# Kernel tuning notes

Measured on AMD Instinct MI355X. Metric: run time of the kernel, lower is better.

## Reference

```python
import jax, jax.numpy as jnp
import numpy as np

TEM = 0.5
BN_EPS = 1e-5
ROWS, IN_FEA, OUT_FEA = 16384, 512, 128


def setup_inputs() -> dict:
    key = jax.random.key(0)
    ks = jax.random.split(key, 3)
    doc_fea = jax.random.normal(ks[0], (ROWS, IN_FEA), dtype=jnp.float32)
    W1 = jax.random.normal(ks[1], (IN_FEA, OUT_FEA), dtype=jnp.float32) * 0.02
    b1 = jnp.zeros((OUT_FEA,), dtype=jnp.float32)
    gamma = jnp.ones((OUT_FEA,), dtype=jnp.float32)
    beta = jnp.zeros((OUT_FEA,), dtype=jnp.float32)
    W2 = jax.random.normal(ks[2], (OUT_FEA, OUT_FEA), dtype=jnp.float32) * 0.02
    b2 = jnp.zeros((OUT_FEA,), dtype=jnp.float32)
    return {"doc_fea": doc_fea, "W1": W1, "b1": b1, "gamma": gamma,
            "beta": beta, "W2": W2, "b2": b2}


def _l2_normalize(x):
    # matches torch F.normalize(dim=1, eps=1e-12)
    n = jnp.linalg.norm(x, axis=1, keepdims=True)
    return x / jnp.maximum(n, 1e-12)


def _half_loss(a, b):
    # rows of a, b are unit-norm, so cosine sim == matmul
    between = jnp.exp(a @ b.T / TEM)          # [N, N]
    refl = jnp.exp(a @ a.T / TEM)             # [N, N]
    pos = jnp.diagonal(between)
    denom = refl.sum(axis=1) + between.sum(axis=1) - jnp.diagonal(refl)
    return -jnp.log(pos / denom)


def reference(doc_fea, W1, b1, gamma, beta, W2, b2):
    # projector: Linear -> BatchNorm1d (training stats) -> ReLU -> Linear
    h = doc_fea @ W1 + b1
    mu = h.mean(axis=0)
    var = h.var(axis=0)  # biased variance, as used by torch BN normalization
    h = (h - mu) * jax.lax.rsqrt(var + BN_EPS) * gamma + beta
    h = jax.nn.relu(h)
    out = h @ W2 + b2
    out = _l2_normalize(out)
    # original: out_1 = out[indices where i%2!=0], out_2 = out[i%2==0]
    out_1 = out[1::2]
    out_2 = out[0::2]
    l1 = _half_loss(out_1, out_2)
    l2 = _half_loss(out_2, out_1)
    loss = (l1 + l2) * 0.5
    return loss.mean()
```

## Files before the change

kernel.cpp:

```cpp
#include <hip/hip_runtime.h>

typedef __attribute__((ext_vector_type(8))) short short8;
typedef __attribute__((ext_vector_type(4))) float f32x4;

typedef const __attribute__((address_space(1))) unsigned int as1_u32;
typedef __attribute__((address_space(3))) unsigned int as3_u32;

#define E2f   7.38905609893065f
#define OSCALE 1.69864357f

#if __has_builtin(__builtin_amdgcn_exp2f)
#define EXP2(x) __builtin_amdgcn_exp2f(x)
#else
#define EXP2(x) exp2f(x)
#endif

__device__ inline unsigned short f2bf(float f){
    union { float f; unsigned int u; } x; x.f = f;
    unsigned int u = x.u;
    return (unsigned short)((u + 0x7fffu + ((u >> 16) & 1u)) >> 16);
}

__device__ inline short8 pack8(float4 a, float4 b){
    short8 t;
    t[0]=(short)f2bf(a.x); t[1]=(short)f2bf(a.y); t[2]=(short)f2bf(a.z); t[3]=(short)f2bf(a.w);
    t[4]=(short)f2bf(b.x); t[5]=(short)f2bf(b.y); t[6]=(short)f2bf(b.z); t[7]=(short)f2bf(b.w);
    return t;
}

__global__ __launch_bounds__(256) void k_prep(const float* __restrict__ W1, const float* __restrict__ W2,
                                              short* __restrict__ W1T, short* __restrict__ W2T){
    int idx = blockIdx.x*256 + threadIdx.x;
    if(idx < 512*128){
        int n = idx >> 9, k = idx & 511;
        W1T[idx] = (short)f2bf(W1[k*128 + n]);
    } else {
        int i2 = idx - 512*128;
        int n = i2 >> 7, k = i2 & 127;
        W2T[i2] = (short)f2bf(W2[k*128 + n]);
    }
}

__global__ __launch_bounds__(256) void k_gemm1(const float* __restrict__ doc, const float* __restrict__ b1,
                                               const short* __restrict__ W1T, float* __restrict__ h,
                                               float* __restrict__ bsum, float* __restrict__ bsq){
    int bid = blockIdx.x;
    int tid = threadIdx.x;
    int w = tid >> 6, l = tid & 63, lr = l & 15, lk = l >> 4;
    int rowA = bid*64 + w*16 + lr;

    short8 a[16];
    const float* dp = doc + rowA*512 + lk*8;
    #pragma unroll
    for(int c=0;c<16;c++){
        float4 f0 = *(const float4*)(dp + c*32);
        float4 f1 = *(const float4*)(dp + c*32 + 4);
        a[c] = pack8(f0, f1);
    }

    f32x4 acc[8];
    #pragma unroll
    for(int ct=0; ct<8; ct++) acc[ct] = (f32x4){0.f,0.f,0.f,0.f};

    const short* wb = W1T + lr*512 + lk*8;
    #pragma unroll
    for(int c=0;c<16;c++){
        #pragma unroll
        for(int ct=0; ct<8; ct++){
            short8 b = *(const short8*)(wb + ct*16*512 + c*32);
            acc[ct] = __builtin_amdgcn_mfma_f32_16x16x32_bf16(a[c], b, acc[ct], 0,0,0);
        }
    }

    __shared__ float lds_s[4][128];
    __shared__ float lds_q[4][128];
    int rowD = bid*64 + w*16 + lk*4;
    #pragma unroll
    for(int ct=0; ct<8; ct++){
        float bb = b1[ct*16 + lr];
        float s = 0.f, q = 0.f;
        #pragma unroll
        for(int r=0;r<4;r++){
            float v = acc[ct][r] + bb;
            h[(rowD + r)*128 + ct*16 + lr] = v;
            s += v; q += v*v;
        }
        s += __shfl_xor(s,16); s += __shfl_xor(s,32);
        q += __shfl_xor(q,16); q += __shfl_xor(q,32);
        if(lk==0){ lds_s[w][ct*16+lr] = s; lds_q[w][ct*16+lr] = q; }
    }
    __syncthreads();
    if(tid < 128){
        float S = lds_s[0][tid]+lds_s[1][tid]+lds_s[2][tid]+lds_s[3][tid];
        float Q = lds_q[0][tid]+lds_q[1][tid]+lds_q[2][tid]+lds_q[3][tid];
        bsum[bid*128 + tid] = S;
        bsq [bid*128 + tid] = Q;
    }
}

__global__ __launch_bounds__(128) void k_bnfin(const float* __restrict__ bsum, const float* __restrict__ bsq,
                                               const float* __restrict__ gamma, const float* __restrict__ beta,
                                               float* __restrict__ bnA, float* __restrict__ bnB){
    int c = threadIdx.x;
    float S=0.f, Q=0.f;
    for(int b=0;b<256;b++){ S += bsum[b*128+c]; Q += bsq[b*128+c]; }
    float mu = S * (1.0f/16384.0f);
    float var = Q * (1.0f/16384.0f) - mu*mu;
    float A = gamma[c] * rsqrtf(var + 1e-5f);
    bnA[c] = A;
    bnB[c] = beta[c] - mu*A;
}

__global__ __launch_bounds__(256) void k_gemm2(const float* __restrict__ h, const short* __restrict__ W2T,
                                               const float* __restrict__ bnA, const float* __restrict__ bnB,
                                               const float* __restrict__ b2,
                                               short* __restrict__ o1s, short* __restrict__ o2s,
                                               float* __restrict__ dvec){
    int bid = blockIdx.x;
    int tid = threadIdx.x;
    int w = tid >> 6, l = tid & 63, lr = l & 15, lk = l >> 4;
    int rowA = bid*64 + w*16 + lr;

    short8 a[4];
    const float* hp = h + rowA*128 + lk*8;
    #pragma unroll
    for(int c=0;c<4;c++){
        float4 h0 = *(const float4*)(hp + c*32);
        float4 h1 = *(const float4*)(hp + c*32 + 4);
        float4 A0 = *(const float4*)(bnA + c*32 + lk*8);
        float4 A1 = *(const float4*)(bnA + c*32 + lk*8 + 4);
        float4 B0 = *(const float4*)(bnB + c*32 + lk*8);
        float4 B1 = *(const float4*)(bnB + c*32 + lk*8 + 4);
        float4 v0, v1;
        v0.x = fmaxf(h0.x*A0.x + B0.x, 0.f); v0.y = fmaxf(h0.y*A0.y + B0.y, 0.f);
        v0.z = fmaxf(h0.z*A0.z + B0.z, 0.f); v0.w = fmaxf(h0.w*A0.w + B0.w, 0.f);
        v1.x = fmaxf(h1.x*A1.x + B1.x, 0.f); v1.y = fmaxf(h1.y*A1.y + B1.y, 0.f);
        v1.z = fmaxf(h1.z*A1.z + B1.z, 0.f); v1.w = fmaxf(h1.w*A1.w + B1.w, 0.f);
        a[c] = pack8(v0, v1);
    }

    f32x4 acc[8];
    #pragma unroll
    for(int ct=0; ct<8; ct++) acc[ct] = (f32x4){0.f,0.f,0.f,0.f};
    const short* wb = W2T + lr*128 + lk*8;
    #pragma unroll
    for(int c=0;c<4;c++){
        #pragma unroll
        for(int ct=0; ct<8; ct++){
            short8 b = *(const short8*)(wb + ct*16*128 + c*32);
            acc[ct] = __builtin_amdgcn_mfma_f32_16x16x32_bf16(a[c], b, acc[ct], 0,0,0);
        }
    }

    #pragma unroll
    for(int ct=0; ct<8; ct++){
        float bb = b2[ct*16 + lr];
        #pragma unroll
        for(int r=0;r<4;r++) acc[ct][r] += bb;
    }
    float n2[4] = {0.f,0.f,0.f,0.f};
    #pragma unroll
    for(int ct=0; ct<8; ct++){
        #pragma unroll
        for(int r=0;r<4;r++) n2[r] += acc[ct][r]*acc[ct][r];
    }
    #pragma unroll
    for(int r=0;r<4;r++){
        n2[r] += __shfl_xor(n2[r],1); n2[r] += __shfl_xor(n2[r],2);
        n2[r] += __shfl_xor(n2[r],4); n2[r] += __shfl_xor(n2[r],8);
    }
    float sc[4];
    #pragma unroll
    for(int r=0;r<4;r++) sc[r] = 1.0f / fmaxf(sqrtf(n2[r]), 1e-12f);
    #pragma unroll
    for(int ct=0; ct<8; ct++){
        #pragma unroll
        for(int r=0;r<4;r++) acc[ct][r] *= sc[r];
    }
    float dp0 = 0.f, dp1 = 0.f;
    #pragma unroll
    for(int ct=0; ct<8; ct++){
        dp0 += acc[ct][0]*acc[ct][1];
        dp1 += acc[ct][2]*acc[ct][3];
    }
    dp0 += __shfl_xor(dp0,1); dp0 += __shfl_xor(dp0,2); dp0 += __shfl_xor(dp0,4); dp0 += __shfl_xor(dp0,8);
    dp1 += __shfl_xor(dp1,1); dp1 += __shfl_xor(dp1,2); dp1 += __shfl_xor(dp1,4); dp1 += __shfl_xor(dp1,8);
    int r0 = bid*64 + w*16 + lk*4;
    if(lr==0){
        dvec[(r0>>1)    ] = dp0;
        dvec[(r0>>1) + 1] = dp1;
    }
    #pragma unroll
    for(int ct=0; ct<8; ct++){
        #pragma unroll
        for(int r=0;r<4;r++){
            int grow = r0 + r;
            int col  = ct*16 + lr;
            short bits = (short)f2bf(acc[ct][r] * OSCALE);
            if(grow & 1) o1s[(grow>>1)*128 + col] = bits;
            else         o2s[(grow>>1)*128 + col] = bits;
        }
    }
}

__global__ __launch_bounds__(256) void k_sim(const short* __restrict__ o1s, const short* __restrict__ o2s,
                                             float* __restrict__ r11p, float* __restrict__ r22p,
                                             float* __restrict__ r12p, float* __restrict__ c12p){
    int bx = blockIdx.x, by = blockIdx.y, pz = blockIdx.z;
    const short* A = (pz==1) ? o2s : o1s;
    const short* B = (pz==0) ? o1s : o2s;
    float* rowp = (pz==0) ? r11p : (pz==1 ? r22p : r12p);
    const bool colsum = (pz==2);

    int tid = threadIdx.x;
    int w = tid>>6, l = tid&63, lr = l&15, lk = l>>4;

    __shared__ __align__(16) short lds[2][8192];
    __shared__ float cs_lds[2][4][64];

    short8 a[2][4];
    {
        const short* ap = A + (bx*128 + w*32 + lr)*128 + lk*8;
        #pragma unroll
        for(int rt=0;rt<2;rt++)
            #pragma unroll
            for(int c=0;c<4;c++)
                a[rt][c] = *(const short8*)(ap + rt*2048 + c*32);
    }

    int sb[4];
    #pragma unroll
    for(int c=0;c<4;c++) sb[c] = lr*256 + ((((c*4+lk) ^ (lr&7)))<<4);

    const short* gsrc[4];
    #pragma unroll
    for(int i=0;i<4;i++){
        int chunk = i*4 + w;
        int row = chunk*4 + (l>>4);
        int col16 = (l&15) ^ (row&7);
        gsrc[i] = B + (by*512 + row)*128 + col16*8;
    }

    #pragma unroll
    for(int i=0;i<4;i++){
        __builtin_amdgcn_global_load_lds((as1_u32*)gsrc[i],
            (as3_u32*)(&lds[0][(i*4+w)*512]), 16, 0, 0);
        gsrc[i] += 8192;
    }
    asm volatile("s_waitcnt vmcnt(0)" ::: "memory");
    __syncthreads();

    float rs[2][4] = {{0.f,0.f,0.f,0.f},{0.f,0.f,0.f,0.f}};
    int buf = 0;
    const char* lbase = (const char*)&lds[0][0];

    for(int t=0;t<8;t++){
        if(t<7){
            #pragma unroll
            for(int i=0;i<4;i++){
                __builtin_amdgcn_global_load_lds((as1_u32*)gsrc[i],
                    (as3_u32*)(&lds[buf^1][(i*4+w)*512]), 16, 0, 0);
                gsrc[i] += 8192;
            }
        }
        const char* lb = lbase + buf*16384;
        #pragma unroll
        for(int jt=0;jt<4;jt++){
            short8 b0 = *(const short8*)(lb + jt*4096 + sb[0]);
            short8 b1 = *(const short8*)(lb + jt*4096 + sb[1]);
            short8 b2 = *(const short8*)(lb + jt*4096 + sb[2]);
            short8 b3 = *(const short8*)(lb + jt*4096 + sb[3]);
            f32x4 c0 = (f32x4){0.f,0.f,0.f,0.f};
            f32x4 c1 = (f32x4){0.f,0.f,0.f,0.f};
            c0 = __builtin_amdgcn_mfma_f32_16x16x32_bf16(a[0][0], b0, c0,0,0,0);
            c1 = __builtin_amdgcn_mfma_f32_16x16x32_bf16(a[1][0], b0, c1,0,0,0);
            c0 = __builtin_amdgcn_mfma_f32_16x16x32_bf16(a[0][1], b1, c0,0,0,0);
            c1 = __builtin_amdgcn_mfma_f32_16x16x32_bf16(a[1][1], b1, c1,0,0,0);
            c0 = __builtin_amdgcn_mfma_f32_16x16x32_bf16(a[0][2], b2, c0,0,0,0);
            c1 = __builtin_amdgcn_mfma_f32_16x16x32_bf16(a[1][2], b2, c1,0,0,0);
            c0 = __builtin_amdgcn_mfma_f32_16x16x32_bf16(a[0][3], b3, c0,0,0,0);
            c1 = __builtin_amdgcn_mfma_f32_16x16x32_bf16(a[1][3], b3, c1,0,0,0);
            float e00 = EXP2(c0[0]), e01 = EXP2(c0[1]), e02 = EXP2(c0[2]), e03 = EXP2(c0[3]);
            float e10 = EXP2(c1[0]), e11 = EXP2(c1[1]), e12 = EXP2(c1[2]), e13 = EXP2(c1[3]);
            rs[0][0]+=e00; rs[0][1]+=e01; rs[0][2]+=e02; rs[0][3]+=e03;
            rs[1][0]+=e10; rs[1][1]+=e11; rs[1][2]+=e12; rs[1][3]+=e13;
            if(colsum){
                float cv = ((e00+e01)+(e02+e03)) + ((e10+e11)+(e12+e13));
                cv += __shfl_xor(cv,16); cv += __shfl_xor(cv,32);
                if(lk==0) cs_lds[t&1][w][jt*16+lr] = cv;
            }
        }
        asm volatile("s_waitcnt vmcnt(0)" ::: "memory");
        __syncthreads();
        if(colsum && tid < 64){
            float v = cs_lds[t&1][0][tid]+cs_lds[t&1][1][tid]
                    + cs_lds[t&1][2][tid]+cs_lds[t&1][3][tid];
            c12p[bx*8192 + by*512 + t*64 + tid] = v;
        }
        buf ^= 1;
    }

    #pragma unroll
    for(int rt=0;rt<2;rt++){
        #pragma unroll
        for(int r=0;r<4;r++){
            rs[rt][r] += __shfl_xor(rs[rt][r],1);
            rs[rt][r] += __shfl_xor(rs[rt][r],2);
            rs[rt][r] += __shfl_xor(rs[rt][r],4);
            rs[rt][r] += __shfl_xor(rs[rt][r],8);
        }
        if(lr==0){
            float4 v; v.x=rs[rt][0]; v.y=rs[rt][1]; v.z=rs[rt][2]; v.w=rs[rt][3];
            *(float4*)(rowp + by*8192 + bx*128 + w*32 + rt*16 + lk*4) = v;
        }
    }
}

__global__ __launch_bounds__(256) void k_loss1(const float* __restrict__ r11, const float* __restrict__ r12,
                                               const float* __restrict__ r22, const float* __restrict__ c12,
                                               const float* __restrict__ dvec, float* __restrict__ lpart){
    int i = blockIdx.x*256 + threadIdx.x;
    float s11=0.f, s12=0.f, s22=0.f, s21=0.f;
    #pragma unroll
    for(int s=0;s<16;s++){
        s11 += r11[s*8192+i]; s12 += r12[s*8192+i]; s22 += r22[s*8192+i];
    }
    #pragma unroll
    for(int s=0;s<64;s++) s21 += c12[s*8192+i];
    float d1 = s11 - E2f + s12;
    float d2 = s22 - E2f + s21;
    float loss = 0.5f*(logf(d1)+logf(d2)) - 2.0f*dvec[i];
    loss += __shfl_xor(loss,1);  loss += __shfl_xor(loss,2);  loss += __shfl_xor(loss,4);
    loss += __shfl_xor(loss,8);  loss += __shfl_xor(loss,16); loss += __shfl_xor(loss,32);
    __shared__ float lds[4];
    if((threadIdx.x & 63) == 0) lds[threadIdx.x >> 6] = loss;
    __syncthreads();
    if(threadIdx.x == 0) lpart[blockIdx.x] = lds[0]+lds[1]+lds[2]+lds[3];
}

__global__ __launch_bounds__(64) void k_loss2(const float* __restrict__ lpart, float* __restrict__ out){
    if(threadIdx.x == 0){
        float s = 0.f;
        for(int i=0;i<32;i++) s += lpart[i];
        out[0] = s * (1.0f/8192.0f);
    }
}

extern "C" void kernel_launch(void* const* d_in, const int* in_sizes, int n_in,
                              void* d_out, int out_size, void* d_ws, size_t ws_size,
                              hipStream_t stream){
    (void)in_sizes; (void)n_in; (void)out_size; (void)ws_size;
    const float* doc   = (const float*)d_in[0];
    const float* W1    = (const float*)d_in[1];
    const float* b1    = (const float*)d_in[2];
    const float* gamma = (const float*)d_in[3];
    const float* beta  = (const float*)d_in[4];
    const float* W2    = (const float*)d_in[5];
    const float* b2    = (const float*)d_in[6];
    float* out = (float*)d_out;

    char* ws = (char*)d_ws;
    float* h     = (float*)(ws + 0);
    float* c12p  = (float*)(ws + 0);
    float* r11p  = (float*)(ws + 2097152);
    float* r22p  = (float*)(ws + 2621440);
    float* r12p  = (float*)(ws + 3145728);
    short* W1T   = (short*)(ws + 8388608);
    short* W2T   = (short*)(ws + 8519680);
    short* o1s   = (short*)(ws + 8552448);
    short* o2s   = (short*)(ws + 10649600);
    float* dvec  = (float*)(ws + 12746752);
    float* bnA   = (float*)(ws + 12779520);
    float* bnB   = (float*)(ws + 12780032);
    float* bsum  = (float*)(ws + 12780544);
    float* bsq   = (float*)(ws + 12911616);
    float* lpart = (float*)(ws + 13042688);

    k_prep <<<320, 256, 0, stream>>>(W1, W2, W1T, W2T);
    k_gemm1<<<256, 256, 0, stream>>>(doc, b1, W1T, h, bsum, bsq);
    k_bnfin<<<1, 128, 0, stream>>>(bsum, bsq, gamma, beta, bnA, bnB);
    k_gemm2<<<256, 256, 0, stream>>>(h, W2T, bnA, bnB, b2, o1s, o2s, dvec);
    dim3 sg(64, 16, 3);
    k_sim  <<<sg, 256, 0, stream>>>(o1s, o2s, r11p, r22p, r12p, c12p);
    k_loss1<<<32, 256, 0, stream>>>(r11p, r12p, r22p, c12p, dvec, lpart);
    k_loss2<<<1, 64, 0, stream>>>(lpart, out);
}
```

Before: 129.1 us.

## Exploit symmetry of self-similarity blocks and restructure GEMM launches and sim pipeline

The similarity kernel now skips lower-triangle tiles of the symmetric a·aᵀ and b·bᵀ matrices. Off-diagonal tiles emit column sums that stand in for the mirrored row sums, and skipped tiles write zeros. Column-sum reduction moves out of the inner loop into registers, and the double-buffered load wait is relaxed to vmcnt(4) with raw barriers. The two projector GEMMs switch to one wave per block with 1024 blocks, with block statistics written directly and reduced by a 512-thread finalize kernel. The EXP2 macro is forced to exp2f. The change trades roughly a third less sim compute for larger column-partial buffers and more reads in the loss kernel.

```diff
diff --git a/kernel.cpp b/kernel.cpp
--- a/kernel.cpp
+++ b/kernel.cpp
@@ -9,11 +9,7 @@
 #define E2f   7.38905609893065f
 #define OSCALE 1.69864357f
 
-#if __has_builtin(__builtin_amdgcn_exp2f)
-#define EXP2(x) __builtin_amdgcn_exp2f(x)
-#else
 #define EXP2(x) exp2f(x)
-#endif
 
 __device__ inline unsigned short f2bf(float f){
     union { float f; unsigned int u; } x; x.f = f;
@@ -41,13 +37,12 @@
     }
 }
 
-__global__ __launch_bounds__(256) void k_gemm1(const float* __restrict__ doc, const float* __restrict__ b1,
-                                               const short* __restrict__ W1T, float* __restrict__ h,
-                                               float* __restrict__ bsum, float* __restrict__ bsq){
+__global__ __launch_bounds__(64) void k_gemm1(const float* __restrict__ doc, const float* __restrict__ b1,
+                                              const short* __restrict__ W1T, float* __restrict__ h,
+                                              float* __restrict__ bsum, float* __restrict__ bsq){
     int bid = blockIdx.x;
-    int tid = threadIdx.x;
-    int w = tid >> 6, l = tid & 63, lr = l & 15, lk = l >> 4;
-    int rowA = bid*64 + w*16 + lr;
+    int l = threadIdx.x, lr = l & 15, lk = l >> 4;
+    int rowA = bid*16 + lr;
 
     short8 a[16];
     const float* dp = doc + rowA*512 + lk*8;
@@ -67,14 +62,12 @@
     for(int c=0;c<16;c++){
         #pragma unroll
         for(int ct=0; ct<8; ct++){
-            short8 b = *(const short8*)(wb + ct*16*512 + c*32);
+            short8 b = *(const short8*)(wb + ct*8192 + c*32);
             acc[ct] = __builtin_amdgcn_mfma_f32_16x16x32_bf16(a[c], b, acc[ct], 0,0,0);
         }
     }
 
-    __shared__ float lds_s[4][128];
-    __shared__ float lds_q[4][128];
-    int rowD = bid*64 + w*16 + lk*4;
+    int rowD = bid*16 + lk*4;
     #pragma unroll
     for(int ct=0; ct<8; ct++){
         float bb = b1[ct*16 + lr];
@@ -87,39 +80,39 @@
         }
         s += __shfl_xor(s,16); s += __shfl_xor(s,32);
         q += __shfl_xor(q,16); q += __shfl_xor(q,32);
-        if(lk==0){ lds_s[w][ct*16+lr] = s; lds_q[w][ct*16+lr] = q; }
-    }
+        if(lk==0){ bsum[bid*128 + ct*16 + lr] = s; bsq[bid*128 + ct*16 + lr] = q; }
+    }
+}
+
+__global__ __launch_bounds__(512) void k_bnfin(const float* __restrict__ bsum, const float* __restrict__ bsq,
+                                               const float* __restrict__ gamma, const float* __restrict__ beta,
+                                               float* __restrict__ bnA, float* __restrict__ bnB){
+    int tid = threadIdx.x;
+    int c = tid & 127, seg = tid >> 7;
+    float S=0.f, Q=0.f;
+    for(int b=seg*256; b<seg*256+256; b++){ S += bsum[b*128+c]; Q += bsq[b*128+c]; }
+    __shared__ float ls[4][128], lq[4][128];
+    ls[seg][c] = S; lq[seg][c] = Q;
     __syncthreads();
     if(tid < 128){
-        float S = lds_s[0][tid]+lds_s[1][tid]+lds_s[2][tid]+lds_s[3][tid];
-        float Q = lds_q[0][tid]+lds_q[1][tid]+lds_q[2][tid]+lds_q[3][tid];
-        bsum[bid*128 + tid] = S;
-        bsq [bid*128 + tid] = Q;
-    }
-}
-
-__global__ __launch_bounds__(128) void k_bnfin(const float* __restrict__ bsum, const float* __restrict__ bsq,
-                                               const float* __restrict__ gamma, const float* __restrict__ beta,
-                                               float* __restrict__ bnA, float* __restrict__ bnB){
-    int c = threadIdx.x;
-    float S=0.f, Q=0.f;
-    for(int b=0;b<256;b++){ S += bsum[b*128+c]; Q += bsq[b*128+c]; }
-    float mu = S * (1.0f/16384.0f);
-    float var = Q * (1.0f/16384.0f) - mu*mu;
-    float A = gamma[c] * rsqrtf(var + 1e-5f);
-    bnA[c] = A;
-    bnB[c] = beta[c] - mu*A;
-}
-
-__global__ __launch_bounds__(256) void k_gemm2(const float* __restrict__ h, const short* __restrict__ W2T,
-                                               const float* __restrict__ bnA, const float* __restrict__ bnB,
-                                               const float* __restrict__ b2,
-                                               short* __restrict__ o1s, short* __restrict__ o2s,
-                                               float* __restrict__ dvec){
+        float St = ls[0][tid]+ls[1][tid]+ls[2][tid]+ls[3][tid];
+        float Qt = lq[0][tid]+lq[1][tid]+lq[2][tid]+lq[3][tid];
+        float mu = St * (1.0f/16384.0f);
+        float var = Qt * (1.0f/16384.0f) - mu*mu;
+        float A = gamma[tid] * rsqrtf(var + 1e-5f);
+        bnA[tid] = A;
+        bnB[tid] = beta[tid] - mu*A;
+    }
+}
+
+__global__ __launch_bounds__(64) void k_gemm2(const float* __restrict__ h, const short* __restrict__ W2T,
+                                              const float* __restrict__ bnA, const float* __restrict__ bnB,
+                                              const float* __restrict__ b2,
+                                              short* __restrict__ o1s, short* __restrict__ o2s,
+                                              float* __restrict__ dvec){
     int bid = blockIdx.x;
-    int tid = threadIdx.x;
-    int w = tid >> 6, l = tid & 63, lr = l & 15, lk = l >> 4;
-    int rowA = bid*64 + w*16 + lr;
+    int l = threadIdx.x, lr = l & 15, lk = l >> 4;
+    int rowA = bid*16 + lr;
 
     short8 a[4];
     const float* hp = h + rowA*128 + lk*8;
@@ -147,7 +140,7 @@
     for(int c=0;c<4;c++){
         #pragma unroll
         for(int ct=0; ct<8; ct++){
-            short8 b = *(const short8*)(wb + ct*16*128 + c*32);
+            short8 b = *(const short8*)(wb + ct*2048 + c*32);
             acc[ct] = __builtin_amdgcn_mfma_f32_16x16x32_bf16(a[c], b, acc[ct], 0,0,0);
         }
     }
@@ -185,7 +178,7 @@
     }
     dp0 += __shfl_xor(dp0,1); dp0 += __shfl_xor(dp0,2); dp0 += __shfl_xor(dp0,4); dp0 += __shfl_xor(dp0,8);
     dp1 += __shfl_xor(dp1,1); dp1 += __shfl_xor(dp1,2); dp1 += __shfl_xor(dp1,4); dp1 += __shfl_xor(dp1,8);
-    int r0 = bid*64 + w*16 + lk*4;
+    int r0 = bid*16 + lk*4;
     if(lr==0){
         dvec[(r0>>1)    ] = dp0;
         dvec[(r0>>1) + 1] = dp1;
@@ -205,18 +198,32 @@
 
 __global__ __launch_bounds__(256) void k_sim(const short* __restrict__ o1s, const short* __restrict__ o2s,
                                              float* __restrict__ r11p, float* __restrict__ r22p,
-                                             float* __restrict__ r12p, float* __restrict__ c12p){
+                                             float* __restrict__ r12p, float* __restrict__ c11p,
+                                             float* __restrict__ c22p, float* __restrict__ c12p){
     int bx = blockIdx.x, by = blockIdx.y, pz = blockIdx.z;
     const short* A = (pz==1) ? o2s : o1s;
     const short* B = (pz==0) ? o1s : o2s;
     float* rowp = (pz==0) ? r11p : (pz==1 ? r22p : r12p);
-    const bool colsum = (pz==2);
+    float* colp = (pz==0) ? c11p : (pz==1 ? c22p : c12p);
 
     int tid = threadIdx.x;
+    int byd = bx >> 2;
+    bool sym = (pz < 2);
+    if(sym && by < byd){
+        if(tid < 128) rowp[by*8192 + bx*128 + tid] = 0.f;
+        colp[bx*8192 + by*512 + tid] = 0.f;
+        colp[bx*8192 + by*512 + 256 + tid] = 0.f;
+        return;
+    }
+    bool do_col = (pz==2) || (by > byd);
+    if(!do_col){
+        colp[bx*8192 + by*512 + tid] = 0.f;
+        colp[bx*8192 + by*512 + 256 + tid] = 0.f;
+    }
+
     int w = tid>>6, l = tid&63, lr = l&15, lk = l>>4;
 
     __shared__ __align__(16) short lds[2][8192];
-    __shared__ float cs_lds[2][4][64];
 
     short8 a[2][4];
     {
@@ -235,8 +242,7 @@
     const short* gsrc[4];
     #pragma unroll
     for(int i=0;i<4;i++){
-        int chunk = i*4 + w;
-        int row = chunk*4 + (l>>4);
+        int row = (i*4 + w)*4 + (l>>4);
         int col16 = (l&15) ^ (row&7);
         gsrc[i] = B + (by*512 + row)*128 + col16*8;
     }
@@ -247,10 +253,9 @@
             (as3_u32*)(&lds[0][(i*4+w)*512]), 16, 0, 0);
         gsrc[i] += 8192;
     }
-    asm volatile("s_waitcnt vmcnt(0)" ::: "memory");
-    __syncthreads();
 
     float rs[2][4] = {{0.f,0.f,0.f,0.f},{0.f,0.f,0.f,0.f}};
+    float cs8[8];
     int buf = 0;
     const char* lbase = (const char*)&lds[0][0];
 
@@ -262,8 +267,14 @@
                     (as3_u32*)(&lds[buf^1][(i*4+w)*512]), 16, 0, 0);
                 gsrc[i] += 8192;
             }
-        }
+            asm volatile("s_waitcnt vmcnt(4)" ::: "memory");
+        } else {
+            asm volatile("s_waitcnt vmcnt(0)" ::: "memory");
+        }
+        __builtin_amdgcn_s_barrier();
+
         const char* lb = lbase + buf*16384;
+        float cst = 0.f;
         #pragma unroll
         for(int jt=0;jt<4;jt++){
             short8 b0 = *(const short8*)(lb + jt*4096 + sb[0]);
@@ -284,19 +295,12 @@
             float e10 = EXP2(c1[0]), e11 = EXP2(c1[1]), e12 = EXP2(c1[2]), e13 = EXP2(c1[3]);
             rs[0][0]+=e00; rs[0][1]+=e01; rs[0][2]+=e02; rs[0][3]+=e03;
             rs[1][0]+=e10; rs[1][1]+=e11; rs[1][2]+=e12; rs[1][3]+=e13;
-            if(colsum){
-                float cv = ((e00+e01)+(e02+e03)) + ((e10+e11)+(e12+e13));
-                cv += __shfl_xor(cv,16); cv += __shfl_xor(cv,32);
-                if(lk==0) cs_lds[t&1][w][jt*16+lr] = cv;
-            }
-        }
-        asm volatile("s_waitcnt vmcnt(0)" ::: "memory");
-        __syncthreads();
-        if(colsum && tid < 64){
-            float v = cs_lds[t&1][0][tid]+cs_lds[t&1][1][tid]
-                    + cs_lds[t&1][2][tid]+cs_lds[t&1][3][tid];
-            c12p[bx*8192 + by*512 + t*64 + tid] = v;
-        }
+            float cv = ((e00+e01)+(e02+e03)) + ((e10+e11)+(e12+e13));
+            cv += __shfl_xor(cv,16); cv += __shfl_xor(cv,32);
+            if(jt == lk) cst = cv;
+        }
+        cs8[t] = cst;
+        __builtin_amdgcn_s_barrier();
         buf ^= 1;
     }
 
@@ -314,19 +318,34 @@
             *(float4*)(rowp + by*8192 + bx*128 + w*32 + rt*16 + lk*4) = v;
         }
     }
-}
-
-__global__ __launch_bounds__(256) void k_loss1(const float* __restrict__ r11, const float* __restrict__ r12,
-                                               const float* __restrict__ r22, const float* __restrict__ c12,
+
+    if(do_col){
+        float* lf = (float*)&lds[0][0];
+        #pragma unroll
+        for(int t=0;t<8;t++) lf[w*512 + t*64 + l] = cs8[t];
+        __syncthreads();
+        int j0 = tid, j1 = tid + 256;
+        float v0 = lf[j0] + lf[512+j0] + lf[1024+j0] + lf[1536+j0];
+        float v1 = lf[j1] + lf[512+j1] + lf[1024+j1] + lf[1536+j1];
+        colp[bx*8192 + by*512 + j0] = v0;
+        colp[bx*8192 + by*512 + j1] = v1;
+    }
+}
+
+__global__ __launch_bounds__(256) void k_loss1(const float* __restrict__ r11, const float* __restrict__ r22,
+                                               const float* __restrict__ r12, const float* __restrict__ c11,
+                                               const float* __restrict__ c22, const float* __restrict__ c12,
                                                const float* __restrict__ dvec, float* __restrict__ lpart){
     int i = blockIdx.x*256 + threadIdx.x;
     float s11=0.f, s12=0.f, s22=0.f, s21=0.f;
     #pragma unroll
     for(int s=0;s<16;s++){
-        s11 += r11[s*8192+i]; s12 += r12[s*8192+i]; s22 += r22[s*8192+i];
-    }
-    #pragma unroll
-    for(int s=0;s<64;s++) s21 += c12[s*8192+i];
+        s11 += r11[s*8192+i]; s22 += r22[s*8192+i]; s12 += r12[s*8192+i];
+    }
+    #pragma unroll
+    for(int s=0;s<64;s++){
+        s11 += c11[s*8192+i]; s22 += c22[s*8192+i]; s21 += c12[s*8192+i];
+    }
     float d1 = s11 - E2f + s12;
     float d2 = s22 - E2f + s21;
     float loss = 0.5f*(logf(d1)+logf(d2)) - 2.0f*dvec[i];
@@ -361,10 +380,12 @@
 
     char* ws = (char*)d_ws;
     float* h     = (float*)(ws + 0);
-    float* c12p  = (float*)(ws + 0);
-    float* r11p  = (float*)(ws + 2097152);
-    float* r22p  = (float*)(ws + 2621440);
-    float* r12p  = (float*)(ws + 3145728);
+    float* c11p  = (float*)(ws + 0);
+    float* c22p  = (float*)(ws + 2097152);
+    float* c12p  = (float*)(ws + 4194304);
+    float* r11p  = (float*)(ws + 6291456);
+    float* r22p  = (float*)(ws + 6815744);
+    float* r12p  = (float*)(ws + 7340032);
     short* W1T   = (short*)(ws + 8388608);
     short* W2T   = (short*)(ws + 8519680);
     short* o1s   = (short*)(ws + 8552448);
@@ -373,15 +394,15 @@
     float* bnA   = (float*)(ws + 12779520);
     float* bnB   = (float*)(ws + 12780032);
     float* bsum  = (float*)(ws + 12780544);
-    float* bsq   = (float*)(ws + 12911616);
-    float* lpart = (float*)(ws + 13042688);
+    float* bsq   = (float*)(ws + 13304832);
+    float* lpart = (float*)(ws + 13829120);
 
     k_prep <<<320, 256, 0, stream>>>(W1, W2, W1T, W2T);
-    k_gemm1<<<256, 256, 0, stream>>>(doc, b1, W1T, h, bsum, bsq);
-    k_bnfin<<<1, 128, 0, stream>>>(bsum, bsq, gamma, beta, bnA, bnB);
-    k_gemm2<<<256, 256, 0, stream>>>(h, W2T, bnA, bnB, b2, o1s, o2s, dvec);
+    k_gemm1<<<1024, 64, 0, stream>>>(doc, b1, W1T, h, bsum, bsq);
+    k_bnfin<<<1, 512, 0, stream>>>(bsum, bsq, gamma, beta, bnA, bnB);
+    k_gemm2<<<1024, 64, 0, stream>>>(h, W2T, bnA, bnB, b2, o1s, o2s, dvec);
     dim3 sg(64, 16, 3);
-    k_sim  <<<sg, 256, 0, stream>>>(o1s, o2s, r11p, r22p, r12p, c12p);
-    k_loss1<<<32, 256, 0, stream>>>(r11p, r12p, r22p, c12p, dvec, lpart);
+    k_sim  <<<sg, 256, 0, stream>>>(o1s, o2s, r11p, r22p, r12p, c11p, c22p, c12p);
+    k_loss1<<<32, 256, 0, stream>>>(r11p, r22p, r12p, c11p, c22p, c12p, dvec, lpart);
     k_loss2<<<1, 64, 0, stream>>>(lpart, out);
 }
```

Result: slower. 234.3 us (+81.5%).
